# Kernel optimization log

Measured on AMD Instinct MI355X. Metric: run time of the kernel, lower is better.

## Reference

```python
import jax, jax.numpy as jnp
import numpy as np

ALPHA = 0.2  # LeakyReLU negative slope
B, N, F, T, H, D = 4, 2048, 256, 8, 4, 64


def setup_inputs() -> dict:
    key = jax.random.key(0)
    ks = jax.random.split(key, 8)
    x = jax.random.normal(ks[0], (B, N, F), dtype=jnp.float32)
    adj = jax.random.randint(ks[1], (B, N, N), 0, 2, dtype=jnp.int32)
    type_idx = jax.random.randint(ks[2], (B, N), 0, T)
    type_onehot = jax.nn.one_hot(type_idx, T, dtype=jnp.float32)
    # per-head parameters stacked on a leading head axis (original uses H separate layers)
    s = 0.06  # ~xavier_uniform scale for these fan sizes
    Wq = jax.random.normal(ks[3], (H, F + T, D), dtype=jnp.float32) * s
    Wk = jax.random.normal(ks[4], (H, F + T, D), dtype=jnp.float32) * s
    W = jax.random.normal(ks[5], (H, F, D), dtype=jnp.float32) * s
    a = jax.random.normal(ks[6], (H, 2 * D, 1), dtype=jnp.float32) * s
    return {"x": x, "adj": adj, "type_onehot": type_onehot,
            "Wq": Wq, "Wk": Wk, "W": W, "a": a}


def reference(x, adj, type_onehot, Wq, Wk, W, a):
    # eval mode: dropout is identity
    nh, d = W.shape[0], W.shape[2]
    h_t = jnp.concatenate([x, type_onehot], axis=-1)           # (B,N,F+T)
    q = jnp.einsum('bnf,hfd->bhnd', h_t, Wq)                   # (B,H,N,D)
    k = jnp.einsum('bnf,hfd->bhnd', h_t, Wk)                   # (B,H,N,D)
    a1 = a[:, :d, 0]                                           # (H,D)
    a2 = a[:, d:, 0]                                           # (H,D)
    e1 = jnp.einsum('bhnd,hd->bhn', q, a1)                     # (B,H,N)
    e2 = jnp.einsum('bhnd,hd->bhn', k, a2)                     # (B,H,N)
    e = e1[:, :, :, None] + e2[:, :, None, :]                  # (B,H,N,N) additive score
    e = jnp.where(e > 0, e, ALPHA * e)                         # leaky relu
    mask = (adj > 0)[:, None, :, :]                            # (B,1,N,N)
    att = jnp.where(mask, e, jnp.float32(-9e15))
    att = jax.nn.softmax(att, axis=2)                          # torch dim=1 of (B,N,N) == axis 2 here
    att = att * adj[:, None, :, :].astype(att.dtype)
    Wh = jnp.einsum('bnf,hfd->bhnd', x, W)                     # (B,H,N,D)
    h_prime = jnp.einsum('bhij,bhjd->bhid', att, Wh)           # (B,H,N,D)
    out = jax.nn.elu(h_prime)                                  # concat=True per head
    # concat heads on feature dim, matching torch.cat([...], dim=2)
    return out.transpose(0, 2, 1, 3).reshape(x.shape[0], x.shape[1], nh * d)
```

## Files before the change

kernel.cpp:

```cpp
#include <hip/hip_runtime.h>
#include <hip/hip_bf16.h>
#include <math.h>

#define ALPHA 0.2f
#define LOG2E 1.4426950408889634f

constexpr int B_ = 4, N_ = 2048, F_ = 256, T_ = 8, H_ = 4, D_ = 64;
constexpr int FT = F_ + T_;

using short8  = __attribute__((ext_vector_type(8))) short;
using float4v = __attribute__((ext_vector_type(4))) float;
using uint4v  = __attribute__((ext_vector_type(4))) unsigned;

#if __has_builtin(__builtin_amdgcn_exp2f)
#define EXP2F(x) __builtin_amdgcn_exp2f(x)
#else
#define EXP2F(x) exp2f(x)
#endif

#define V1_OFF    0u
#define V2_OFF    4224u
#define E1A_OFF   8448u
#define E2A_OFF   270592u
#define PC_OFF    532736u
#define NC_OFF    663808u
#define PARTS_OFF 794880u
#define WT_OFF    2892032u
#define BITS_OFF  3023104u
#define WHT_OFF   5120256u

__device__ inline unsigned short f2bf_rne(float f) {
    unsigned u = __builtin_bit_cast(unsigned, f);
    u += 0x7FFFu + ((u >> 16) & 1u);
    return (unsigned short)(u >> 16);
}
__device__ inline unsigned pack_bf_rne(float f0, float f1) {
    return (unsigned)f2bf_rne(f0) | ((unsigned)f2bf_rne(f1) << 16);
}
__device__ inline unsigned pack_bf_trunc(float f0, float f1) {
    unsigned u0 = __builtin_bit_cast(unsigned, f0);
    unsigned u1 = __builtin_bit_cast(unsigned, f1);
    return (u0 >> 16) | (u1 & 0xFFFF0000u);
}
__device__ inline void gl2lds16(const void* g, void* l) {
    __builtin_amdgcn_global_load_lds(
        (const __attribute__((address_space(1))) unsigned*)g,
        (__attribute__((address_space(3))) unsigned*)l, 16, 0, 0);
}

__global__ __launch_bounds__(256) void k_adjpack(const int* __restrict__ adj,
                                                 unsigned* __restrict__ bits) {
    size_t tid = (size_t)blockIdx.x * 256 + threadIdx.x;
    int av = adj[tid];
    unsigned long long msk = __ballot(av != 0);
    int lane = threadIdx.x & 63;
    if (lane == 0)       bits[tid >> 5] = (unsigned)msk;
    else if (lane == 32) bits[tid >> 5] = (unsigned)(msk >> 32);
}

__global__ __launch_bounds__(256) void k_prep_v(const float* __restrict__ Wq,
                                                const float* __restrict__ Wk,
                                                const float* __restrict__ a,
                                                float* __restrict__ v1,
                                                float* __restrict__ v2) {
    int tid = blockIdx.x * 256 + threadIdx.x;
    if (tid >= 2 * H_ * FT) return;
    int sel = tid / (H_ * FT);
    int r = tid - sel * (H_ * FT);
    int h = r / FT, f = r - h * FT;
    const float* W = sel ? Wk : Wq;
    const float* av = a + h * 2 * D_ + sel * D_;
    const float* wrow = W + (size_t)(h * FT + f) * D_;
    float acc = 0.f;
    for (int d = 0; d < D_; ++d) acc += wrow[d] * av[d];
    (sel ? v2 : v1)[h * FT + f] = acc * LOG2E;
}

__global__ __launch_bounds__(256) void k_prep_wt(const float* __restrict__ W,
                                                 unsigned short* __restrict__ WT) {
    int tid = blockIdx.x * 256 + threadIdx.x;
    int hd = tid >> 8, f = tid & 255;
    int h = hd >> 6, d = hd & 63;
    WT[(size_t)hd * F_ + f] = f2bf_rne(W[((size_t)h * F_ + f) * D_ + d]);
}

__global__ __launch_bounds__(256) void k_e12(const float* __restrict__ x,
                                             const float* __restrict__ oh,
                                             const float* __restrict__ v1,
                                             const float* __restrict__ v2,
                                             float2* __restrict__ E1A,
                                             float2* __restrict__ E2A) {
    int lane = threadIdx.x & 63;
    int w = threadIdx.x >> 6;
    int bn = blockIdx.x * 4 + w;
    int b = bn >> 11, n = bn & (N_ - 1);
    float a1h[H_] = {0.f, 0.f, 0.f, 0.f};
    float a2h[H_] = {0.f, 0.f, 0.f, 0.f};
    const float* xrow = x + (size_t)(b * N_ + n) * F_;
    for (int c = 0; c < 4; ++c) {
        int f = c * 64 + lane;
        float xv = xrow[f];
        #pragma unroll
        for (int h = 0; h < H_; ++h) {
            a1h[h] += xv * v1[h * FT + f];
            a2h[h] += xv * v2[h * FT + f];
        }
    }
    if (lane < T_) {
        float ov = oh[(size_t)(b * N_ + n) * T_ + lane];
        #pragma unroll
        for (int h = 0; h < H_; ++h) {
            a1h[h] += ov * v1[h * FT + F_ + lane];
            a2h[h] += ov * v2[h * FT + F_ + lane];
        }
    }
    #pragma unroll
    for (int off = 32; off; off >>= 1) {
        #pragma unroll
        for (int h = 0; h < H_; ++h) {
            a1h[h] += __shfl_xor(a1h[h], off, 64);
            a2h[h] += __shfl_xor(a2h[h], off, 64);
        }
    }
    if (lane == 0) {
        #pragma unroll
        for (int h = 0; h < H_; ++h) {
            float2 v1o = {EXP2F(a1h[h]), EXP2F(ALPHA * a1h[h])};
            float2 v2o = {EXP2F(a2h[h]), EXP2F(ALPHA * a2h[h])};
            E1A[(size_t)(b * H_ + h) * N_ + n] = v1o;
            E2A[(size_t)(b * H_ + h) * N_ + n] = v2o;
        }
    }
}

__global__ __launch_bounds__(256) void k_wht(const float* __restrict__ x,
                                             const unsigned short* __restrict__ WT,
                                             unsigned short* __restrict__ WhT) {
    int lane = threadIdx.x;
    int h = threadIdx.y;
    int jt = blockIdx.x;
    int b  = blockIdx.y;
    int j0 = jt * 16;
    int m = lane & 15, quad = lane >> 4;
    float4v zero = {0.f, 0.f, 0.f, 0.f};
    float4v acc[4] = {zero, zero, zero, zero};
    #pragma unroll 2
    for (int f0 = 0; f0 < F_; f0 += 32) {
        const float* xp = x + (size_t)(b * N_ + j0 + m) * F_ + f0 + quad * 8;
        float4v xlo = *(const float4v*)xp;
        float4v xhi = *(const float4v*)(xp + 4);
        uint4v bp = {pack_bf_rne(xlo[0], xlo[1]), pack_bf_rne(xlo[2], xlo[3]),
                     pack_bf_rne(xhi[0], xhi[1]), pack_bf_rne(xhi[2], xhi[3])};
        short8 bfrag = __builtin_bit_cast(short8, bp);
        #pragma unroll
        for (int mt = 0; mt < 4; ++mt) {
            const unsigned short* ap =
                WT + (size_t)(h * 64 + mt * 16 + m) * F_ + f0 + quad * 8;
            short8 afrag = *(const short8*)ap;
            acc[mt] = __builtin_amdgcn_mfma_f32_16x16x32_bf16(afrag, bfrag, acc[mt], 0, 0, 0);
        }
    }
    #pragma unroll
    for (int mt = 0; mt < 4; ++mt) {
        #pragma unroll
        for (int reg = 0; reg < 4; ++reg) {
            int hd = h * 64 + mt * 16 + quad * 4 + reg;
            WhT[((size_t)b * 256 + hd) * N_ + j0 + m] = f2bf_rne(acc[mt][reg]);
        }
    }
}

__global__ __launch_bounds__(256) void k_colsum(const unsigned* __restrict__ bits,
                                                const float2* __restrict__ E1A,
                                                const float2* __restrict__ E2A,
                                                float* __restrict__ part_s) {
    int tid = threadIdx.x;
    int jt = blockIdx.x, b = blockIdx.y, ic = blockIdx.z;
    int j = jt * 256 + tid;
    int i0 = ic * 128;
    float2 e2v[H_];
    float acc[H_] = {0.f, 0.f, 0.f, 0.f};
    #pragma unroll
    for (int h = 0; h < H_; ++h) e2v[h] = E2A[(size_t)(b * H_ + h) * N_ + j];
    const float2* e1b = E1A + (size_t)(b * H_) * N_;
    const unsigned* bp = bits + ((size_t)(b * N_ + i0)) * 64 + (j >> 5);
    unsigned sh = j & 31;
    #pragma unroll 8
    for (int k = 0; k < 128; ++k) {
        unsigned wv = bp[(size_t)k * 64];
        bool on = (wv >> sh) & 1u;
        int i = i0 + k;
        #pragma unroll
        for (int h = 0; h < H_; ++h) {
            float2 e1 = e1b[h * N_ + i];
            float t = fmaxf(e1.x * e2v[h].x, e1.y * e2v[h].y);
            acc[h] += on ? t : 0.f;
        }
    }
    #pragma unroll
    for (int h = 0; h < H_; ++h)
        part_s[(size_t)ic * (B_ * H_ * N_) + (size_t)(b * H_ + h) * N_ + j] = acc[h];
}

__global__ __launch_bounds__(256) void k_scale(const float* __restrict__ part_s,
                                               const float2* __restrict__ E2A,
                                               float* __restrict__ pc,
                                               float* __restrict__ nc) {
    int tid = blockIdx.x * 256 + threadIdx.x;
    float s = 0.f;
    #pragma unroll
    for (int ic = 0; ic < 16; ++ic) s += part_s[(size_t)ic * (B_ * H_ * N_) + tid];
    float c = (s > 0.f) ? 1.f / s : 0.f;
    float2 e2 = E2A[tid];
    pc[tid] = e2.x * c;
    nc[tid] = e2.y * c;
}

__global__ __launch_bounds__(512, 4) void k_main(const unsigned* __restrict__ bits,
                                                 const float2* __restrict__ E1A,
                                                 const float* __restrict__ pc_g,
                                                 const float* __restrict__ nc_g,
                                                 const unsigned short* __restrict__ WhT,
                                                 float* __restrict__ out) {
    __shared__ float sPC[2048];
    __shared__ float sNC[2048];
    __shared__ unsigned short sW[2][2][4096];
    int lane = threadIdx.x;
    int wy = threadIdx.y;
    int iT = wy & 3, hf = wy >> 2;
    int it = blockIdx.x;
    int b  = blockIdx.y;
    int h  = blockIdx.z;
    int ibase = it * 64 + iT * 16;
    int m = lane & 15, quad = lane >> 4;
    int bh = b * H_ + h;

    {
        int base = (wy * 64 + lane) * 4;
        *(float4v*)&sPC[base] = *(const float4v*)(pc_g + (size_t)bh * N_ + base);
        *(float4v*)&sNC[base] = *(const float4v*)(nc_g + (size_t)bh * N_ + base);
    }
    float2 e1v = E1A[(size_t)bh * N_ + ibase + m];
    const unsigned short* bbase = WhT + (size_t)(b * 256 + h * 64) * N_;
    const unsigned* brow = bits + ((size_t)(b * N_) + ibase + m) * 64 + hf * 32;

    auto stage = [&](int buf, int jb) {
        #pragma unroll
        for (int s2 = 0; s2 < 2; ++s2) {
            int phi = s2 * 256 + iT * 64 + lane;
            int r = phi >> 3, sg = phi & 7;
            int g = sg ^ (r & 7);
            const unsigned short* gp = bbase + (size_t)r * N_ + hf * 1024 + jb + g * 8;
            void* lp = (void*)&sW[hf][buf][(s2 * 256 + iT * 64) * 8];
            gl2lds16(gp, lp);
        }
    };

    stage(0, 0);
    __syncthreads();

    float4v zero = {0.f, 0.f, 0.f, 0.f};
    float4v acc[4] = {zero, zero, zero, zero};
    uint4v bw = {0, 0, 0, 0};

    for (int k = 0; k < 16; ++k) {
        if (k < 15) stage((k + 1) & 1, (k + 1) * 64);
        if ((k & 1) == 0) bw = *(const uint4v*)(brow + k * 2);
        #pragma unroll
        for (int u = 0; u < 2; ++u) {
            int t = 2 * k + u;
            unsigned word = bw[(k & 1) * 2 + u];
            unsigned wq = word >> (quad * 8);
            int jl = hf * 1024 + t * 32 + quad * 8;
            float4v p0 = *(const float4v*)&sPC[jl];
            float4v p1 = *(const float4v*)&sPC[jl + 4];
            float4v n0 = *(const float4v*)&sNC[jl];
            float4v n1 = *(const float4v*)&sNC[jl + 4];
            float w[8];
            #pragma unroll
            for (int e = 0; e < 4; ++e) {
                float t1 = fmaxf(e1v.x * p0[e], e1v.y * n0[e]);
                w[e] = (wq & (1u << e)) ? t1 : 0.f;
            }
            #pragma unroll
            for (int e = 0; e < 4; ++e) {
                float t1 = fmaxf(e1v.x * p1[e], e1v.y * n1[e]);
                w[4 + e] = (wq & (16u << e)) ? t1 : 0.f;
            }
            uint4v apk = {pack_bf_trunc(w[0], w[1]), pack_bf_trunc(w[2], w[3]),
                          pack_bf_trunc(w[4], w[5]), pack_bf_trunc(w[6], w[7])};
            short8 afrag = __builtin_bit_cast(short8, apk);
            #pragma unroll
            for (int dt = 0; dt < 4; ++dt) {
                int r = dt * 16 + m;
                int seg = (u * 4 + quad) ^ (m & 7);
                short8 bfrag = *(const short8*)&sW[hf][k & 1][r * 64 + seg * 8];
                acc[dt] = __builtin_amdgcn_mfma_f32_16x16x32_bf16(afrag, bfrag, acc[dt], 0, 0, 0);
            }
        }
        __syncthreads();
    }

    float* sRed = (float*)&sW[0][0][0];
    #pragma unroll
    for (int dt = 0; dt < 4; ++dt)
        #pragma unroll
        for (int reg = 0; reg < 4; ++reg)
            sRed[wy * 1024 + (dt * 4 + reg) * 64 + lane] = acc[dt][reg];
    __syncthreads();

    int tt = wy * 64 + lane;
    #pragma unroll
    for (int s = 0; s < 8; ++s) {
        int v = s * 512 + tt;
        float val = sRed[v] + sRed[4096 + v];
        val = val > 0.f ? val : expm1f(val);
        int iT2 = v >> 10, rr = (v >> 6) & 15, l = v & 63;
        int dt = rr >> 2, reg = rr & 3;
        int i = it * 64 + iT2 * 16 + (l >> 4) * 4 + reg;
        int d = dt * 16 + (l & 15);
        out[((size_t)(b * N_ + i)) * (H_ * D_) + h * D_ + d] = val;
    }
}

extern "C" void kernel_launch(void* const* d_in, const int* in_sizes, int n_in,
                              void* d_out, int out_size, void* d_ws, size_t ws_size,
                              hipStream_t stream) {
    const float* x   = (const float*)d_in[0];
    const int*   adj = (const int*)d_in[1];
    const float* oh  = (const float*)d_in[2];
    const float* Wq  = (const float*)d_in[3];
    const float* Wk  = (const float*)d_in[4];
    const float* W   = (const float*)d_in[5];
    const float* a   = (const float*)d_in[6];
    float* out = (float*)d_out;
    char* ws = (char*)d_ws;

    float*  v1    = (float*)(ws + V1_OFF);
    float*  v2    = (float*)(ws + V2_OFF);
    float2* E1A   = (float2*)(ws + E1A_OFF);
    float2* E2A   = (float2*)(ws + E2A_OFF);
    float*  pc    = (float*)(ws + PC_OFF);
    float*  nc    = (float*)(ws + NC_OFF);
    float*  parts = (float*)(ws + PARTS_OFF);
    unsigned short* WT   = (unsigned short*)(ws + WT_OFF);
    unsigned*       bits = (unsigned*)(ws + BITS_OFF);
    unsigned short* WhT  = (unsigned short*)(ws + WHT_OFF);

    k_adjpack<<<65536, 256, 0, stream>>>(adj, bits);
    k_prep_v<<<9, 256, 0, stream>>>(Wq, Wk, a, v1, v2);
    k_prep_wt<<<256, 256, 0, stream>>>(W, WT);
    k_e12<<<B_ * N_ / 4, 256, 0, stream>>>(x, oh, v1, v2, E1A, E2A);
    k_wht<<<dim3(128, 4), dim3(64, 4), 0, stream>>>(x, WT, WhT);
    k_colsum<<<dim3(8, 4, 16), 256, 0, stream>>>(bits, E1A, E2A, parts);
    k_scale<<<128, 256, 0, stream>>>(parts, E2A, pc, nc);
    k_main<<<dim3(32, 4, 4), dim3(64, 8), 0, stream>>>(bits, E1A, pc, nc, WhT, out);
}
```

Baseline: 192.7 us.

## Switch to fp16 MFMA, LUT-based masking, and drop the split-j reduction in main kernel

Replaces bf16 with fp16 throughout: packing uses cvt_pkrtz and the MFMAs become f16 variants. The main kernel drops from 8 waves with a two-way j split and shared-memory reduction to 4 waves that each cover the full j range. Each wave stages 128-column tiles of Wh with a 16-way XOR swizzle and applies the adjacency mask through a shared LUT that is ANDed onto the packed halves. The two small prep kernels are merged into one launch. Risks are fp16 range and precision loss for large attention weights, and half as many waves per block in the main kernel.

```diff
diff --git a/kernel.cpp b/kernel.cpp
--- a/kernel.cpp
+++ b/kernel.cpp
@@ -8,7 +8,8 @@
 constexpr int B_ = 4, N_ = 2048, F_ = 256, T_ = 8, H_ = 4, D_ = 64;
 constexpr int FT = F_ + T_;
 
-using short8  = __attribute__((ext_vector_type(8))) short;
+using half8   = __attribute__((ext_vector_type(8))) _Float16;
+using half2v  = __attribute__((ext_vector_type(2))) _Float16;
 using float4v = __attribute__((ext_vector_type(4))) float;
 using uint4v  = __attribute__((ext_vector_type(4))) unsigned;
 
@@ -17,6 +18,10 @@
 #else
 #define EXP2F(x) exp2f(x)
 #endif
+
+__device__ inline unsigned pkrtz_u(float a, float b) {
+    return __builtin_bit_cast(unsigned, __builtin_amdgcn_cvt_pkrtz(a, b));
+}
 
 #define V1_OFF    0u
 #define V2_OFF    4224u
@@ -29,19 +34,6 @@
 #define BITS_OFF  3023104u
 #define WHT_OFF   5120256u
 
-__device__ inline unsigned short f2bf_rne(float f) {
-    unsigned u = __builtin_bit_cast(unsigned, f);
-    u += 0x7FFFu + ((u >> 16) & 1u);
-    return (unsigned short)(u >> 16);
-}
-__device__ inline unsigned pack_bf_rne(float f0, float f1) {
-    return (unsigned)f2bf_rne(f0) | ((unsigned)f2bf_rne(f1) << 16);
-}
-__device__ inline unsigned pack_bf_trunc(float f0, float f1) {
-    unsigned u0 = __builtin_bit_cast(unsigned, f0);
-    unsigned u1 = __builtin_bit_cast(unsigned, f1);
-    return (u0 >> 16) | (u1 & 0xFFFF0000u);
-}
 __device__ inline void gl2lds16(const void* g, void* l) {
     __builtin_amdgcn_global_load_lds(
         (const __attribute__((address_space(1))) unsigned*)g,
@@ -58,30 +50,31 @@
     else if (lane == 32) bits[tid >> 5] = (unsigned)(msk >> 32);
 }
 
-__global__ __launch_bounds__(256) void k_prep_v(const float* __restrict__ Wq,
-                                                const float* __restrict__ Wk,
-                                                const float* __restrict__ a,
-                                                float* __restrict__ v1,
-                                                float* __restrict__ v2) {
-    int tid = blockIdx.x * 256 + threadIdx.x;
+__global__ __launch_bounds__(256) void k_prep(const float* __restrict__ Wq,
+                                              const float* __restrict__ Wk,
+                                              const float* __restrict__ a,
+                                              const float* __restrict__ W,
+                                              float* __restrict__ v1,
+                                              float* __restrict__ v2,
+                                              _Float16* __restrict__ WT) {
+    int gid = blockIdx.x * 256 + threadIdx.x;
+    if (gid < 65536) {
+        int hd = gid >> 8, f = gid & 255;
+        int h = hd >> 6, d = hd & 63;
+        WT[(size_t)hd * F_ + f] = (_Float16)W[((size_t)h * F_ + f) * D_ + d];
+        return;
+    }
+    int tid = gid - 65536;
     if (tid >= 2 * H_ * FT) return;
     int sel = tid / (H_ * FT);
     int r = tid - sel * (H_ * FT);
     int h = r / FT, f = r - h * FT;
-    const float* W = sel ? Wk : Wq;
+    const float* Wx = sel ? Wk : Wq;
     const float* av = a + h * 2 * D_ + sel * D_;
-    const float* wrow = W + (size_t)(h * FT + f) * D_;
+    const float* wrow = Wx + (size_t)(h * FT + f) * D_;
     float acc = 0.f;
     for (int d = 0; d < D_; ++d) acc += wrow[d] * av[d];
     (sel ? v2 : v1)[h * FT + f] = acc * LOG2E;
-}
-
-__global__ __launch_bounds__(256) void k_prep_wt(const float* __restrict__ W,
-                                                 unsigned short* __restrict__ WT) {
-    int tid = blockIdx.x * 256 + threadIdx.x;
-    int hd = tid >> 8, f = tid & 255;
-    int h = hd >> 6, d = hd & 63;
-    WT[(size_t)hd * F_ + f] = f2bf_rne(W[((size_t)h * F_ + f) * D_ + d]);
 }
 
 __global__ __launch_bounds__(256) void k_e12(const float* __restrict__ x,
@@ -125,17 +118,16 @@
     if (lane == 0) {
         #pragma unroll
         for (int h = 0; h < H_; ++h) {
-            float2 v1o = {EXP2F(a1h[h]), EXP2F(ALPHA * a1h[h])};
-            float2 v2o = {EXP2F(a2h[h]), EXP2F(ALPHA * a2h[h])};
-            E1A[(size_t)(b * H_ + h) * N_ + n] = v1o;
-            E2A[(size_t)(b * H_ + h) * N_ + n] = v2o;
+            size_t o = (size_t)(b * H_ + h) * N_ + n;
+            E1A[o] = {EXP2F(a1h[h]), EXP2F(ALPHA * a1h[h])};
+            E2A[o] = {EXP2F(a2h[h]), EXP2F(ALPHA * a2h[h])};
         }
     }
 }
 
 __global__ __launch_bounds__(256) void k_wht(const float* __restrict__ x,
-                                             const unsigned short* __restrict__ WT,
-                                             unsigned short* __restrict__ WhT) {
+                                             const _Float16* __restrict__ WT,
+                                             _Float16* __restrict__ WhT) {
     int lane = threadIdx.x;
     int h = threadIdx.y;
     int jt = blockIdx.x;
@@ -149,15 +141,14 @@
         const float* xp = x + (size_t)(b * N_ + j0 + m) * F_ + f0 + quad * 8;
         float4v xlo = *(const float4v*)xp;
         float4v xhi = *(const float4v*)(xp + 4);
-        uint4v bp = {pack_bf_rne(xlo[0], xlo[1]), pack_bf_rne(xlo[2], xlo[3]),
-                     pack_bf_rne(xhi[0], xhi[1]), pack_bf_rne(xhi[2], xhi[3])};
-        short8 bfrag = __builtin_bit_cast(short8, bp);
+        uint4v bp = {pkrtz_u(xlo[0], xlo[1]), pkrtz_u(xlo[2], xlo[3]),
+                     pkrtz_u(xhi[0], xhi[1]), pkrtz_u(xhi[2], xhi[3])};
+        half8 bfrag = __builtin_bit_cast(half8, bp);
         #pragma unroll
         for (int mt = 0; mt < 4; ++mt) {
-            const unsigned short* ap =
-                WT + (size_t)(h * 64 + mt * 16 + m) * F_ + f0 + quad * 8;
-            short8 afrag = *(const short8*)ap;
-            acc[mt] = __builtin_amdgcn_mfma_f32_16x16x32_bf16(afrag, bfrag, acc[mt], 0, 0, 0);
+            const _Float16* ap = WT + (size_t)(h * 64 + mt * 16 + m) * F_ + f0 + quad * 8;
+            half8 afrag = *(const half8*)ap;
+            acc[mt] = __builtin_amdgcn_mfma_f32_16x16x32_f16(afrag, bfrag, acc[mt], 0, 0, 0);
         }
     }
     #pragma unroll
@@ -165,7 +156,7 @@
         #pragma unroll
         for (int reg = 0; reg < 4; ++reg) {
             int hd = h * 64 + mt * 16 + quad * 4 + reg;
-            WhT[((size_t)b * 256 + hd) * N_ + j0 + m] = f2bf_rne(acc[mt][reg]);
+            WhT[((size_t)b * 256 + hd) * N_ + j0 + m] = (_Float16)acc[mt][reg];
         }
     }
 }
@@ -216,42 +207,49 @@
     nc[tid] = e2.y * c;
 }
 
-__global__ __launch_bounds__(512, 4) void k_main(const unsigned* __restrict__ bits,
+__global__ __launch_bounds__(256, 2) void k_main(const unsigned* __restrict__ bits,
                                                  const float2* __restrict__ E1A,
                                                  const float* __restrict__ pc_g,
                                                  const float* __restrict__ nc_g,
-                                                 const unsigned short* __restrict__ WhT,
+                                                 const _Float16* __restrict__ WhT,
                                                  float* __restrict__ out) {
     __shared__ float sPC[2048];
     __shared__ float sNC[2048];
-    __shared__ unsigned short sW[2][2][4096];
+    __shared__ unsigned sLUT[256][4];
+    __shared__ _Float16 sW[2][8192];
     int lane = threadIdx.x;
     int wy = threadIdx.y;
-    int iT = wy & 3, hf = wy >> 2;
     int it = blockIdx.x;
     int b  = blockIdx.y;
     int h  = blockIdx.z;
-    int ibase = it * 64 + iT * 16;
+    int ibase = it * 64 + wy * 16;
     int m = lane & 15, quad = lane >> 4;
     int bh = b * H_ + h;
+    int t256 = wy * 64 + lane;
 
     {
-        int base = (wy * 64 + lane) * 4;
-        *(float4v*)&sPC[base] = *(const float4v*)(pc_g + (size_t)bh * N_ + base);
-        *(float4v*)&sNC[base] = *(const float4v*)(nc_g + (size_t)bh * N_ + base);
+        unsigned t = t256;
+        sLUT[t][0] = ((t & 1u) ? 0xFFFFu : 0u) | ((t & 2u) ? 0xFFFF0000u : 0u);
+        sLUT[t][1] = ((t & 4u) ? 0xFFFFu : 0u) | ((t & 8u) ? 0xFFFF0000u : 0u);
+        sLUT[t][2] = ((t & 16u) ? 0xFFFFu : 0u) | ((t & 32u) ? 0xFFFF0000u : 0u);
+        sLUT[t][3] = ((t & 64u) ? 0xFFFFu : 0u) | ((t & 128u) ? 0xFFFF0000u : 0u);
+        int base = t256 * 8;
+        *(float4v*)&sPC[base]     = *(const float4v*)(pc_g + (size_t)bh * N_ + base);
+        *(float4v*)&sPC[base + 4] = *(const float4v*)(pc_g + (size_t)bh * N_ + base + 4);
+        *(float4v*)&sNC[base]     = *(const float4v*)(nc_g + (size_t)bh * N_ + base);
+        *(float4v*)&sNC[base + 4] = *(const float4v*)(nc_g + (size_t)bh * N_ + base + 4);
     }
     float2 e1v = E1A[(size_t)bh * N_ + ibase + m];
-    const unsigned short* bbase = WhT + (size_t)(b * 256 + h * 64) * N_;
-    const unsigned* brow = bits + ((size_t)(b * N_) + ibase + m) * 64 + hf * 32;
+    const _Float16* bbase = WhT + (size_t)(b * 256 + h * 64) * N_;
+    const unsigned* brow = bits + ((size_t)(b * N_) + ibase + m) * 64;
 
     auto stage = [&](int buf, int jb) {
         #pragma unroll
-        for (int s2 = 0; s2 < 2; ++s2) {
-            int phi = s2 * 256 + iT * 64 + lane;
-            int r = phi >> 3, sg = phi & 7;
-            int g = sg ^ (r & 7);
-            const unsigned short* gp = bbase + (size_t)r * N_ + hf * 1024 + jb + g * 8;
-            void* lp = (void*)&sW[hf][buf][(s2 * 256 + iT * 64) * 8];
+        for (int q = 0; q < 4; ++q) {
+            int r = q * 16 + wy * 4 + (lane >> 4);
+            int g = (lane & 15) ^ (r & 15);
+            const _Float16* gp = bbase + (size_t)r * N_ + jb + g * 8;
+            void* lp = (void*)&sW[buf][q * 2048 + wy * 512];
             gl2lds16(gp, lp);
         }
     };
@@ -261,65 +259,48 @@
 
     float4v zero = {0.f, 0.f, 0.f, 0.f};
     float4v acc[4] = {zero, zero, zero, zero};
-    uint4v bw = {0, 0, 0, 0};
 
     for (int k = 0; k < 16; ++k) {
-        if (k < 15) stage((k + 1) & 1, (k + 1) * 64);
-        if ((k & 1) == 0) bw = *(const uint4v*)(brow + k * 2);
-        #pragma unroll
-        for (int u = 0; u < 2; ++u) {
-            int t = 2 * k + u;
-            unsigned word = bw[(k & 1) * 2 + u];
-            unsigned wq = word >> (quad * 8);
-            int jl = hf * 1024 + t * 32 + quad * 8;
-            float4v p0 = *(const float4v*)&sPC[jl];
-            float4v p1 = *(const float4v*)&sPC[jl + 4];
-            float4v n0 = *(const float4v*)&sNC[jl];
-            float4v n1 = *(const float4v*)&sNC[jl + 4];
+        if (k < 15) stage((k + 1) & 1, (k + 1) * 128);
+        uint4v bwv = *(const uint4v*)(brow + k * 4);
+        #pragma unroll
+        for (int u = 0; u < 4; ++u) {
+            unsigned byte = (bwv[u] >> (quad * 8)) & 0xFFu;
+            uint4v msk = *(const uint4v*)&sLUT[byte][0];
+            int jg = k * 128 + u * 32 + quad * 8;
+            float4v p0 = *(const float4v*)&sPC[jg];
+            float4v p1 = *(const float4v*)&sPC[jg + 4];
+            float4v n0 = *(const float4v*)&sNC[jg];
+            float4v n1 = *(const float4v*)&sNC[jg + 4];
             float w[8];
             #pragma unroll
-            for (int e = 0; e < 4; ++e) {
-                float t1 = fmaxf(e1v.x * p0[e], e1v.y * n0[e]);
-                w[e] = (wq & (1u << e)) ? t1 : 0.f;
-            }
+            for (int e = 0; e < 4; ++e) w[e]     = fmaxf(e1v.x * p0[e], e1v.y * n0[e]);
             #pragma unroll
-            for (int e = 0; e < 4; ++e) {
-                float t1 = fmaxf(e1v.x * p1[e], e1v.y * n1[e]);
-                w[4 + e] = (wq & (16u << e)) ? t1 : 0.f;
-            }
-            uint4v apk = {pack_bf_trunc(w[0], w[1]), pack_bf_trunc(w[2], w[3]),
-                          pack_bf_trunc(w[4], w[5]), pack_bf_trunc(w[6], w[7])};
-            short8 afrag = __builtin_bit_cast(short8, apk);
+            for (int e = 0; e < 4; ++e) w[4 + e] = fmaxf(e1v.x * p1[e], e1v.y * n1[e]);
+            uint4v wvp = {pkrtz_u(w[0], w[1]) & msk[0], pkrtz_u(w[2], w[3]) & msk[1],
+                          pkrtz_u(w[4], w[5]) & msk[2], pkrtz_u(w[6], w[7]) & msk[3]};
+            half8 afrag = __builtin_bit_cast(half8, wvp);
             #pragma unroll
             for (int dt = 0; dt < 4; ++dt) {
                 int r = dt * 16 + m;
-                int seg = (u * 4 + quad) ^ (m & 7);
-                short8 bfrag = *(const short8*)&sW[hf][k & 1][r * 64 + seg * 8];
-                acc[dt] = __builtin_amdgcn_mfma_f32_16x16x32_bf16(afrag, bfrag, acc[dt], 0, 0, 0);
+                int segp = (u * 4 + quad) ^ m;
+                half8 bfrag = *(const half8*)&sW[k & 1][r * 128 + segp * 8];
+                acc[dt] = __builtin_amdgcn_mfma_f32_16x16x32_f16(afrag, bfrag, acc[dt], 0, 0, 0);
             }
         }
         __syncthreads();
     }
 
-    float* sRed = (float*)&sW[0][0][0];
-    #pragma unroll
-    for (int dt = 0; dt < 4; ++dt)
-        #pragma unroll
-        for (int reg = 0; reg < 4; ++reg)
-            sRed[wy * 1024 + (dt * 4 + reg) * 64 + lane] = acc[dt][reg];
-    __syncthreads();
-
-    int tt = wy * 64 + lane;
-    #pragma unroll
-    for (int s = 0; s < 8; ++s) {
-        int v = s * 512 + tt;
-        float val = sRed[v] + sRed[4096 + v];
-        val = val > 0.f ? val : expm1f(val);
-        int iT2 = v >> 10, rr = (v >> 6) & 15, l = v & 63;
-        int dt = rr >> 2, reg = rr & 3;
-        int i = it * 64 + iT2 * 16 + (l >> 4) * 4 + reg;
-        int d = dt * 16 + (l & 15);
-        out[((size_t)(b * N_ + i)) * (H_ * D_) + h * D_ + d] = val;
+    #pragma unroll
+    for (int dt = 0; dt < 4; ++dt) {
+        #pragma unroll
+        for (int reg = 0; reg < 4; ++reg) {
+            int i = ibase + quad * 4 + reg;
+            int d = dt * 16 + m;
+            float v = acc[dt][reg];
+            v = v > 0.f ? v : expm1f(v);
+            out[((size_t)(b * N_ + i)) * (H_ * D_) + h * D_ + d] = v;
+        }
     }
 }
 
@@ -336,23 +317,22 @@
     float* out = (float*)d_out;
     char* ws = (char*)d_ws;
 
-    float*  v1    = (float*)(ws + V1_OFF);
-    float*  v2    = (float*)(ws + V2_OFF);
-    float2* E1A   = (float2*)(ws + E1A_OFF);
-    float2* E2A   = (float2*)(ws + E2A_OFF);
-    float*  pc    = (float*)(ws + PC_OFF);
-    float*  nc    = (float*)(ws + NC_OFF);
-    float*  parts = (float*)(ws + PARTS_OFF);
-    unsigned short* WT   = (unsigned short*)(ws + WT_OFF);
-    unsigned*       bits = (unsigned*)(ws + BITS_OFF);
-    unsigned short* WhT  = (unsigned short*)(ws + WHT_OFF);
+    float*   v1    = (float*)(ws + V1_OFF);
+    float*   v2    = (float*)(ws + V2_OFF);
+    float2*  E1A   = (float2*)(ws + E1A_OFF);
+    float2*  E2A   = (float2*)(ws + E2A_OFF);
+    float*   pc    = (float*)(ws + PC_OFF);
+    float*   nc    = (float*)(ws + NC_OFF);
+    float*   parts = (float*)(ws + PARTS_OFF);
+    _Float16* WT   = (_Float16*)(ws + WT_OFF);
+    unsigned* bits = (unsigned*)(ws + BITS_OFF);
+    _Float16* WhT  = (_Float16*)(ws + WHT_OFF);
 
     k_adjpack<<<65536, 256, 0, stream>>>(adj, bits);
-    k_prep_v<<<9, 256, 0, stream>>>(Wq, Wk, a, v1, v2);
-    k_prep_wt<<<256, 256, 0, stream>>>(W, WT);
+    k_prep<<<265, 256, 0, stream>>>(Wq, Wk, a, W, v1, v2, WT);
     k_e12<<<B_ * N_ / 4, 256, 0, stream>>>(x, oh, v1, v2, E1A, E2A);
     k_wht<<<dim3(128, 4), dim3(64, 4), 0, stream>>>(x, WT, WhT);
     k_colsum<<<dim3(8, 4, 16), 256, 0, stream>>>(bits, E1A, E2A, parts);
     k_scale<<<128, 256, 0, stream>>>(parts, E2A, pc, nc);
-    k_main<<<dim3(32, 4, 4), dim3(64, 8), 0, stream>>>(bits, E1A, pc, nc, WhT, out);
-}
+    k_main<<<dim3(32, 4, 4), dim3(64, 4), 0, stream>>>(bits, E1A, pc, nc, WhT, out);
+}
```

Measured after the change: 185.5 us. 3.7% less time.
